# Kernel tuning notes

Hardware: AMD Instinct MI355X
Metric: run time of the kernel (lower is better)

Reference implementation:

```python
import jax, jax.numpy as jnp
import numpy as np

B, L, D_MODEL = 8, 2048, 768
D_INNER, D_STATE, DT_RANK, K = 1536, 16, 48, 4


def setup_inputs() -> dict:
    key = jax.random.key(0)
    ks = jax.random.split(key, 9)
    s = 0.02
    return {
        "hidden_states": jax.random.normal(ks[0], (B, L, D_MODEL), jnp.float32),
        "W_in": jax.random.normal(ks[1], (D_MODEL, 2 * D_INNER), jnp.float32) * s,
        "conv_w": jax.random.normal(ks[2], (D_INNER, 1, K), jnp.float32) * s,
        "conv_b": jax.random.normal(ks[3], (D_INNER,), jnp.float32) * s,
        "W_x": jax.random.normal(ks[4], (DT_RANK + 2 * D_STATE, D_INNER), jnp.float32) * s,
        "W_dt": jax.random.normal(ks[5], (D_INNER, DT_RANK), jnp.float32) * s,
        "b_dt": jax.random.normal(ks[6], (D_INNER,), jnp.float32) * s,
        "A_log": jax.random.normal(ks[7], (D_INNER, D_STATE), jnp.float32),
        "D_param": jax.random.normal(ks[8], (D_INNER,), jnp.float32),
    }


def _mamba(hidden_states, W_in, conv_w, conv_b, W_x, W_dt, b_dt, A_log, D_param):
    # in_proj then chunk into ssm branch (x) and gating residual (res)
    xz = hidden_states @ W_in                      # (B, L, 2*d_inner)
    x, res = jnp.split(xz, 2, axis=-1)             # each (B, L, d_inner)

    # causal depthwise conv over time, then SiLU
    xc = x.transpose(0, 2, 1)                      # (B, C, L)
    xc = jax.lax.conv_general_dilated(
        xc, conv_w, window_strides=(1,), padding=[(K - 1, 0)],
        feature_group_count=D_INNER, dimension_numbers=("NCH", "OIH", "NCH"))
    x = jax.nn.silu(xc + conv_b[None, :, None]).transpose(0, 2, 1)  # (B, L, d_inner)

    # input-dependent SSM parameters
    x_dbl = x @ W_x.T                              # (B, L, dt_rank + 2*d_state)
    dt = jax.nn.softplus(x_dbl[..., :DT_RANK] @ W_dt.T + b_dt)      # (B, L, d_inner)
    Bm = x_dbl[..., DT_RANK:DT_RANK + D_STATE]     # (B, L, d_state)
    Cm = x_dbl[..., DT_RANK + D_STATE:]            # (B, L, d_state)
    A = -jnp.exp(A_log)                            # (d_inner, d_state)

    def step(h, inp):
        x_t, dt_t, B_t, C_t = inp                  # (B,d_inner),(B,d_inner),(B,d_state),(B,d_state)
        dA = jnp.exp(dt_t[..., None] * A)          # (B, d_inner, d_state)
        dBx = (dt_t * x_t)[..., None] * B_t[:, None, :]
        h = dA * h + dBx
        y = jnp.einsum("bds,bs->bd", h, C_t)
        return h, y

    xs = (x.transpose(1, 0, 2), dt.transpose(1, 0, 2),
          Bm.transpose(1, 0, 2), Cm.transpose(1, 0, 2))
    h0 = jnp.zeros((x.shape[0], D_INNER, D_STATE), x.dtype)
    _, ys = jax.lax.scan(step, h0, xs)             # ys: (L, B, d_inner)
    y = ys.transpose(1, 0, 2) + x * D_param        # skip term
    return y * jax.nn.silu(res)                    # gated output (B, L, d_inner)


def reference(hidden_states, W_in, conv_w, conv_b, W_x, W_dt, b_dt, A_log, D_param):
    return _mamba(hidden_states, W_in, conv_w, conv_b, W_x, W_dt, b_dt, A_log, D_param)
```

## Files before the change

### kernel.cpp

```cpp
#include <hip/hip_runtime.h>
#include <hip/hip_bf16.h>
#include <stdint.h>

#define B_SZ 8
#define L_SZ 2048
#define DM 768
#define DI 1536
#define DS 16
#define DR 48
#define M_SZ (B_SZ * L_SZ)
#define N1 (2 * DI)

#define NC 32
#define TC (L_SZ / NC)
#define CH (B_SZ * DI)
#define KS 6
#define NT2 (DM / 32)
#define L2E 1.44269504088896f

typedef short short8 __attribute__((ext_vector_type(8)));
typedef float f32x4 __attribute__((ext_vector_type(4)));
typedef float f32x2 __attribute__((ext_vector_type(2)));

__device__ __forceinline__ ushort f2b(float f) {
  __hip_bfloat16 h = __float2bfloat16(f);
  return *reinterpret_cast<ushort*>(&h);
}
__device__ __forceinline__ float b2f(ushort u) {
  __hip_bfloat16 h;
  *reinterpret_cast<ushort*>(&h) = u;
  return __bfloat162float(h);
}
__device__ __forceinline__ ushort f2h(float f) {
  _Float16 h = (_Float16)f;
  return *reinterpret_cast<ushort*>(&h);
}
__device__ __forceinline__ float h2f(ushort u) {
  _Float16 h;
  *reinterpret_cast<ushort*>(&h) = u;
  return (float)h;
}

__device__ __forceinline__ void gl16(const ushort* g, ushort* l) {
  __builtin_amdgcn_global_load_lds(
      (const __attribute__((address_space(1))) void*)g,
      (__attribute__((address_space(3))) void*)l, 16, 0, 0);
}


__global__ __launch_bounds__(256) void prep_all(const float4* __restrict__ hs4,
                                                const float* __restrict__ w_in,
                                                const float* __restrict__ wx_f,
                                                const float* __restrict__ wdt_f,
                                                ushort4* __restrict__ A1,
                                                ushort* __restrict__ wt,
                                                ushort* __restrict__ wx_b,
                                                ushort* __restrict__ wdt_p) {
  const int n4 = M_SZ * DM / 4;
  const int nT = 3072 * 96;
  const int nwx = 80 * DI;
  const int nwdt = DI * 64;
  int idx = blockIdx.x * 256 + threadIdx.x;
  if (idx < n4) {
    float4 v = hs4[idx];
    ushort4 o;
    o.x = f2b(v.x); o.y = f2b(v.y); o.z = f2b(v.z); o.w = f2b(v.w);
    A1[idx] = o;
  } else if (idx < n4 + nT) {
    int j = idx - n4;
    int n = j % 3072;
    int kb = (j / 3072) * 8;
    short8 o;
#pragma unroll
    for (int q = 0; q < 8; ++q) o[q] = (short)f2b(w_in[(size_t)(kb + q) * 3072 + n]);
    *(short8*)(wt + (size_t)n * DM + kb) = o;
  } else if (idx < n4 + nT + nwx) {
    int j = idx - n4 - nT;
    wx_b[j] = f2b(wx_f[j]);
  } else if (idx < n4 + nT + nwx + nwdt) {
    int j = idx - n4 - nT - nwx;
    int col = j >> 6, k = j & 63;
    wdt_p[j] = (k < DR) ? f2b(wdt_f[col * DR + k]) : (ushort)0;
  }
}


__global__ __launch_bounds__(512, 4) void gemm_xz(const ushort* __restrict__ A,
                                                  const ushort* __restrict__ Bt,
                                                  ushort* __restrict__ xout,
                                                  ushort* __restrict__ gateout) {
  __shared__ ushort lds[36864];

  const int t = threadIdx.x;
  const int lane = t & 63;
  const int wid = t >> 6;
  const int wm = wid >> 2, wn = wid & 3;
  const int r = lane & 15, hi = lane >> 4;

  const int g = blockIdx.x;
  const int swz = (g & 7) * 192 + (g >> 3);
  const int bx = swz & 63;
  const int by = swz >> 6;
  const int bm = bx * 256;
  const int bn = by * 128;

  const ushort* gsrc[3];
  int ldso[3];
#pragma unroll
  for (int i = 0; i < 3; ++i) {
    int c = wid * 3 + i;
    if (c < 16)
      gsrc[i] = A + (size_t)(bm + c * 16 + r) * DM + hi * 8;
    else
      gsrc[i] = Bt + (size_t)(bn + (c - 16) * 16 + r) * DM + hi * 8;
    ldso[i] = c * 512;
  }

  f32x4 acc[8][2];
#pragma unroll
  for (int m = 0; m < 8; ++m)
#pragma unroll
    for (int n = 0; n < 2; ++n) acc[m][n] = f32x4{0.f, 0.f, 0.f, 0.f};

  ushort* b0 = lds;
  ushort* b1 = lds + 12288;
  ushort* b2 = lds + 24576;

#pragma unroll
  for (int i = 0; i < 3; ++i) gl16(gsrc[i], b0 + ldso[i]);
#pragma unroll
  for (int i = 0; i < 3; ++i) gl16(gsrc[i] + 32, b1 + ldso[i]);
  asm volatile("s_waitcnt vmcnt(3)" ::: "memory");
  __builtin_amdgcn_s_barrier();

  for (int kt = 0; kt < NT2; ++kt) {
    const bool stage = (kt + 2 < NT2);
    const int koff = (kt + 2) * 32;

    short8 bfr[2];
#pragma unroll
    for (int n = 0; n < 2; ++n)
      bfr[n] = *(const short8*)&b0[(16 + wn * 2 + n) * 512 + lane * 8];

#pragma unroll
    for (int q = 0; q < 2; ++q) {
      short8 afr[4];
#pragma unroll
      for (int m = 0; m < 4; ++m)
        afr[m] = *(const short8*)&b0[(wm * 8 + q * 4 + m) * 512 + lane * 8];

      if (stage) {
        if (q == 0) {
          gl16(gsrc[0] + koff, b2 + ldso[0]);
          gl16(gsrc[1] + koff, b2 + ldso[1]);
        } else {
          gl16(gsrc[2] + koff, b2 + ldso[2]);
        }
      }

      asm volatile("s_barrier" ::: "memory");

      __builtin_amdgcn_s_setprio(1);
#pragma unroll
      for (int m = 0; m < 4; ++m)
#pragma unroll
        for (int n = 0; n < 2; ++n)
          acc[q * 4 + m][n] =
              __builtin_amdgcn_mfma_f32_16x16x32_bf16(afr[m], bfr[n], acc[q * 4 + m][n], 0, 0, 0);
      __builtin_amdgcn_s_setprio(0);

      if (q == 1) {
        if (stage)
          asm volatile("s_waitcnt vmcnt(3)" ::: "memory");
        else
          asm volatile("s_waitcnt vmcnt(0)" ::: "memory");
      }
      asm volatile("s_barrier" ::: "memory");
    }

    ushort* tmp = b0; b0 = b1; b1 = b2; b2 = tmp;
  }

  const bool isx = (bn < DI);
  ushort* outp = isx ? xout : gateout;
  const int cbase = bn - (isx ? 0 : DI) + wn * 32;
#pragma unroll
  for (int mf = 0; mf < 8; ++mf)
#pragma unroll
    for (int nf = 0; nf < 2; ++nf) {
      int col = cbase + nf * 16 + r;
#pragma unroll
      for (int j = 0; j < 4; ++j) {
        int row = bm + wm * 128 + mf * 16 + hi * 4 + j;
        float v = acc[mf][nf][j];
        if (!isx) v = v / (1.f + __expf(-v));
        outp[(size_t)row * DI + col] = f2b(v);
      }
    }
}


__global__ __launch_bounds__(256) void conv_silu(const ushort* __restrict__ xp,
                                                 const float* __restrict__ cw,
                                                 const float* __restrict__ cb,
                                                 ushort* __restrict__ xc) {
  int tid = blockIdx.x * 256 + threadIdx.x;
  const int nd = DI / 8;
  int db = tid % nd;
  int row = tid / nd;
  int d0 = db * 8;
  int l = row & (L_SZ - 1);
  const ushort* base = xp + (size_t)row * DI + d0;
  short8 z8 = {0, 0, 0, 0, 0, 0, 0, 0};
  short8 x0 = *(const short8*)base;
  short8 xm1 = (l >= 1) ? *(const short8*)(base - DI) : z8;
  short8 xm2 = (l >= 2) ? *(const short8*)(base - 2 * DI) : z8;
  short8 xm3 = (l >= 3) ? *(const short8*)(base - 3 * DI) : z8;
  short8 o;
#pragma unroll
  for (int j = 0; j < 8; ++j) {
    float4 w = *(const float4*)(cw + (size_t)(d0 + j) * 4);
    float a = cb[d0 + j] + w.x * b2f((ushort)xm3[j]) + w.y * b2f((ushort)xm2[j]) +
              w.z * b2f((ushort)xm1[j]) + w.w * b2f((ushort)x0[j]);
    float s = a / (1.f + __expf(-a));
    o[j] = (short)f2b(s);
  }
  *(short8*)(xc + (size_t)row * DI + d0) = o;
}


__global__ __launch_bounds__(256) void xdbl_gemm(const ushort* __restrict__ xc,
                                                 const ushort* __restrict__ wx,
                                                 float* __restrict__ xdp) {
  int wave = blockIdx.x * 4 + (threadIdx.x >> 6);
  int ks = blockIdx.y;
  int lane = threadIdx.x & 63;
  int r = lane & 15, hi = lane >> 4;
  int row0 = wave * 16;
  f32x4 acc[5];
#pragma unroll
  for (int n = 0; n < 5; ++n) acc[n] = f32x4{0.f, 0.f, 0.f, 0.f};
  const int kbeg = ks * (DI / KS), kend = kbeg + DI / KS;
  for (int k0 = kbeg; k0 < kend; k0 += 32) {
    short8 a = *(const short8*)(xc + (size_t)(row0 + r) * DI + k0 + hi * 8);
#pragma unroll
    for (int n = 0; n < 5; ++n) {
      short8 b = *(const short8*)(wx + (size_t)(n * 16 + r) * DI + k0 + hi * 8);
      acc[n] = __builtin_amdgcn_mfma_f32_16x16x32_bf16(a, b, acc[n], 0, 0, 0);
    }
  }
  float* op = xdp + (size_t)ks * M_SZ * 80;
#pragma unroll
  for (int n = 0; n < 5; ++n)
#pragma unroll
    for (int j = 0; j < 4; ++j)
      op[(size_t)(row0 + hi * 4 + j) * 80 + n * 16 + r] = acc[n][j];
}

__global__ __launch_bounds__(256) void reduce_xd(const float4* __restrict__ xdp,
                                                 float4* __restrict__ xd) {
  int i = blockIdx.x * 256 + threadIdx.x;
  if (i >= M_SZ * 20) return;
  float4 s = xdp[i];
#pragma unroll
  for (int k = 1; k < KS; ++k) {
    float4 v = xdp[(size_t)k * M_SZ * 20 + i];
    s.x += v.x; s.y += v.y; s.z += v.z; s.w += v.w;
  }
  xd[i] = s;
}


__device__ __forceinline__ short8 pack8f(const float* p) {
  short8 v;
#pragma unroll
  for (int i = 0; i < 8; ++i) v[i] = (short)f2b(p[i]);
  return v;
}

__global__ __launch_bounds__(256) void dt_gemm(const float* __restrict__ xd,
                                               const ushort* __restrict__ wdtp,
                                               const float* __restrict__ bdt,
                                               ushort* __restrict__ dt) {
  int wave = blockIdx.x * 4 + (threadIdx.x >> 6);
  int lane = threadIdx.x & 63;
  int r = lane & 15, hi = lane >> 4;
  int row0 = wave * 16;
  int c0 = blockIdx.y * 64;

  float atmp[8];
  const float* ap = xd + (size_t)(row0 + r) * 80 + hi * 8;
  float4 q0 = *(const float4*)ap, q1 = *(const float4*)(ap + 4);
  atmp[0] = q0.x; atmp[1] = q0.y; atmp[2] = q0.z; atmp[3] = q0.w;
  atmp[4] = q1.x; atmp[5] = q1.y; atmp[6] = q1.z; atmp[7] = q1.w;
  short8 a0 = pack8f(atmp);
  short8 a1 = {0, 0, 0, 0, 0, 0, 0, 0};
  if (hi < 2) {
    const float* ap1 = xd + (size_t)(row0 + r) * 80 + 32 + hi * 8;
    float4 p0 = *(const float4*)ap1, p1 = *(const float4*)(ap1 + 4);
    atmp[0] = p0.x; atmp[1] = p0.y; atmp[2] = p0.z; atmp[3] = p0.w;
    atmp[4] = p1.x; atmp[5] = p1.y; atmp[6] = p1.z; atmp[7] = p1.w;
    a1 = pack8f(atmp);
  }

  f32x4 acc[4];
#pragma unroll
  for (int n = 0; n < 4; ++n) acc[n] = f32x4{0.f, 0.f, 0.f, 0.f};
#pragma unroll
  for (int n = 0; n < 4; ++n) {
    const ushort* wp = wdtp + (size_t)(c0 + n * 16 + r) * 64;
    short8 b0 = *(const short8*)(wp + hi * 8);
    short8 b1 = *(const short8*)(wp + 32 + hi * 8);
    acc[n] = __builtin_amdgcn_mfma_f32_16x16x32_bf16(a0, b0, acc[n], 0, 0, 0);
    acc[n] = __builtin_amdgcn_mfma_f32_16x16x32_bf16(a1, b1, acc[n], 0, 0, 0);
  }
#pragma unroll
  for (int n = 0; n < 4; ++n)
#pragma unroll
    for (int j = 0; j < 4; ++j) {
      int col = c0 + n * 16 + r;
      float z = acc[n][j] + bdt[col];
      float sp = (z > 20.f) ? z : __logf(1.f + __expf(z));
      dt[(size_t)(row0 + hi * 4 + j) * DI + col] = f2h(sp);
    }
}


__global__ __launch_bounds__(256) void scan_pass1(const ushort* __restrict__ dt,
                                                  const ushort* __restrict__ xc,
                                                  const float* __restrict__ xd,
                                                  const float* __restrict__ A_log,
                                                  float* __restrict__ hend,
                                                  float* __restrict__ sumdt) {
  const int d = blockIdx.x * 256 + threadIdx.x;
  const int c = blockIdx.y, b = blockIdx.z;
  const int t0 = c * TC;

  __shared__ float Bs[TC * 16];
  for (int i = threadIdx.x; i < TC * 16; i += 256) {
    int tt = i >> 4, s = i & 15;
    Bs[i] = xd[((size_t)(b * L_SZ + t0 + tt)) * 80 + DR + s];
  }

  f32x2 a2[8];
  const float4* al4 = (const float4*)(A_log + (size_t)d * DS);
#pragma unroll
  for (int q = 0; q < 4; ++q) {
    float4 v = al4[q];
    a2[2 * q] = f32x2{-__expf(v.x) * L2E, -__expf(v.y) * L2E};
    a2[2 * q + 1] = f32x2{-__expf(v.z) * L2E, -__expf(v.w) * L2E};
  }

  __syncthreads();

  f32x2 h2[8];
#pragma unroll
  for (int q = 0; q < 8; ++q) h2[q] = f32x2{0.f, 0.f};
  float sd = 0.f;

  const ushort* dtp = dt + ((size_t)b * L_SZ + t0) * DI + d;
  const ushort* xp = xc + ((size_t)b * L_SZ + t0) * DI + d;

  ushort dtu_n = *dtp;
  ushort xu_n = *xp;
  const f32x2* bp2 = (const f32x2*)Bs;
#pragma unroll 2
  for (int tt = 0; tt < TC; ++tt) {
    dtp += DI; xp += DI;
    ushort dtu = dtu_n;
    ushort xu = xu_n;
    dtu_n = *dtp;
    xu_n = *xp;
    float dtv = h2f(dtu);
    float xv = b2f(xu);
    sd += dtv;
    float dx = dtv * xv;
    f32x2 dts = f32x2{dtv, dtv};
    f32x2 dxs = f32x2{dx, dx};
#pragma unroll
    for (int q = 0; q < 8; ++q) {
      f32x2 bv = bp2[q];
      f32x2 arg, t2;
      asm("v_pk_mul_f32 %0, %1, %2" : "=v"(arg) : "v"(dts), "v"(a2[q]));
      float e0, e1;
      asm("v_exp_f32 %0, %1" : "=v"(e0) : "v"(arg[0]));
      asm("v_exp_f32 %0, %1" : "=v"(e1) : "v"(arg[1]));
      asm("v_pk_mul_f32 %0, %1, %2" : "=v"(t2) : "v"(dxs), "v"(bv));
      h2[q][0] = __builtin_fmaf(e0, h2[q][0], t2[0]);
      h2[q][1] = __builtin_fmaf(e1, h2[q][1], t2[1]);
    }
    bp2 += 8;
  }

  const size_t ch = (size_t)b * DI + d;
  sumdt[ch * NC + c] = sd;
  f32x2* hp = (f32x2*)&hend[((size_t)c * CH + ch) * 16];
#pragma unroll
  for (int q = 0; q < 8; ++q) hp[q] = h2[q];
}

__global__ __launch_bounds__(256) void scan_pass2(const float* __restrict__ A_log,
                                                  const float* __restrict__ sumdt,
                                                  const float* __restrict__ hend,
                                                  float* __restrict__ hstart) {
  int idx = blockIdx.x * 256 + threadIdx.x;
  int ch = idx >> 4, s = idx & 15;
  int d = ch % DI;
  float A = -__expf(A_log[d * DS + s]);
  float h = 0.f;
  for (int c = 0; c < NC; ++c) {
    hstart[((size_t)c * CH + ch) * 16 + s] = h;
    float sd = sumdt[(size_t)ch * NC + c];
    h = __expf(A * sd) * h + hend[((size_t)c * CH + ch) * 16 + s];
  }
}

__global__ __launch_bounds__(256) void scan_pass3(const ushort* __restrict__ dt,
                                                  const ushort* __restrict__ xc,
                                                  const float* __restrict__ xd,
                                                  const ushort* __restrict__ gateb,
                                                  const float* __restrict__ A_log,
                                                  const float* __restrict__ Dp,
                                                  const float* __restrict__ hstart,
                                                  float* __restrict__ out) {
  const int d = blockIdx.x * 256 + threadIdx.x;
  const int c = blockIdx.y, b = blockIdx.z;
  const int t0 = c * TC;

  __shared__ float Bs[TC * 16];
  __shared__ float Cs[TC * 16];
  for (int i = threadIdx.x; i < TC * 16; i += 256) {
    int tt = i >> 4, s = i & 15;
    size_t row = ((size_t)(b * L_SZ + t0 + tt)) * 80;
    Bs[i] = xd[row + DR + s];
    Cs[i] = xd[row + DR + DS + s];
  }

  f32x2 a2[8];
  const float4* al4 = (const float4*)(A_log + (size_t)d * DS);
#pragma unroll
  for (int q = 0; q < 4; ++q) {
    float4 v = al4[q];
    a2[2 * q] = f32x2{-__expf(v.x) * L2E, -__expf(v.y) * L2E};
    a2[2 * q + 1] = f32x2{-__expf(v.z) * L2E, -__expf(v.w) * L2E};
  }
  const float Dpv = Dp[d];

  const size_t ch = (size_t)b * DI + d;
  f32x2 h2[8];
  const f32x2* hp = (const f32x2*)&hstart[((size_t)c * CH + ch) * 16];
#pragma unroll
  for (int q = 0; q < 8; ++q) h2[q] = hp[q];

  __syncthreads();

  const ushort* dtp = dt + ((size_t)b * L_SZ + t0) * DI + d;
  const ushort* xp = xc + ((size_t)b * L_SZ + t0) * DI + d;
  const ushort* gp = gateb + ((size_t)b * L_SZ + t0) * DI + d;
  float* op = out + ((size_t)b * L_SZ + t0) * DI + d;

  ushort dtu_n = *dtp;
  ushort xu_n = *xp;
  ushort gu_n = *gp;
  const f32x2* bp2 = (const f32x2*)Bs;
  const f32x2* cp2 = (const f32x2*)Cs;
#pragma unroll 2
  for (int tt = 0; tt < TC; ++tt) {
    dtp += DI; xp += DI; gp += DI;
    ushort dtu = dtu_n;
    ushort xu = xu_n;
    ushort gu = gu_n;
    dtu_n = *dtp;
    xu_n = *xp;
    gu_n = *gp;
    float dtv = h2f(dtu);
    float xv = b2f(xu);
    float gv = b2f(gu);
    float dx = dtv * xv;
    f32x2 dts = f32x2{dtv, dtv};
    f32x2 dxs = f32x2{dx, dx};
    f32x2 ya = f32x2{0.f, 0.f}, yb = f32x2{0.f, 0.f};
#pragma unroll
    for (int q = 0; q < 8; ++q) {
      f32x2 bv = bp2[q];
      f32x2 cv = cp2[q];
      f32x2 arg, t2;
      asm("v_pk_mul_f32 %0, %1, %2" : "=v"(arg) : "v"(dts), "v"(a2[q]));
      float e0, e1;
      asm("v_exp_f32 %0, %1" : "=v"(e0) : "v"(arg[0]));
      asm("v_exp_f32 %0, %1" : "=v"(e1) : "v"(arg[1]));
      asm("v_pk_mul_f32 %0, %1, %2" : "=v"(t2) : "v"(dxs), "v"(bv));
      h2[q][0] = __builtin_fmaf(e0, h2[q][0], t2[0]);
      h2[q][1] = __builtin_fmaf(e1, h2[q][1], t2[1]);
      if (q & 1)
        asm("v_pk_fma_f32 %0, %1, %2, %0" : "+v"(yb) : "v"(h2[q]), "v"(cv));
      else
        asm("v_pk_fma_f32 %0, %1, %2, %0" : "+v"(ya) : "v"(h2[q]), "v"(cv));
    }
    bp2 += 8; cp2 += 8;
    float y = (ya[0] + ya[1]) + (yb[0] + yb[1]);
    op[0] = (y + xv * Dpv) * gv;
    op += DI;
  }
}


extern "C" void kernel_launch(void* const* d_in, const int* in_sizes, int n_in,
                              void* d_out, int out_size, void* d_ws, size_t ws_size,
                              hipStream_t stream) {
  const float* hs     = (const float*)d_in[0];
  const float* W_in   = (const float*)d_in[1];
  const float* conv_w = (const float*)d_in[2];
  const float* conv_b = (const float*)d_in[3];
  const float* W_x    = (const float*)d_in[4];
  const float* W_dt   = (const float*)d_in[5];
  const float* b_dt   = (const float*)d_in[6];
  const float* A_log  = (const float*)d_in[7];
  const float* D_par  = (const float*)d_in[8];
  float* out = (float*)d_out;
  char* ws = (char*)d_ws;

  size_t o = 0;
  ushort* A1   = (ushort*)(ws + o); o += (size_t)M_SZ * DM * 2;
  ushort* Wt1  = (ushort*)(ws + o); o += (size_t)N1 * DM * 2;
  ushort* xpre = (ushort*)(ws + o); o += (size_t)M_SZ * DI * 2;
  ushort* gate = (ushort*)(ws + o); o += (size_t)M_SZ * DI * 2;
  ushort* xcv  = (ushort*)(ws + o); o += (size_t)M_SZ * DI * 2;
  float*  xdbl = (float*)(ws + o);  o += (size_t)M_SZ * 80 * 4;
  ushort* dtb  = (ushort*)(ws + o); o += (size_t)M_SZ * DI * 2;
  float*  xdp  = (float*)(ws + o);  o += (size_t)KS * M_SZ * 80 * 4;
  ushort* Wxb  = (ushort*)(ws + o); o += (size_t)80 * DI * 2;
  ushort* Wdtp = (ushort*)(ws + o); o += (size_t)DI * 64 * 2;
  if (ws_size < o) return;

  float* hend   = (float*)(ws + 0);
  float* hstart = (float*)(ws + (size_t)NC * CH * 16 * 4);
  float* sumdt  = (float*)(ws + (size_t)2 * NC * CH * 16 * 4);

  const int nprep = M_SZ * DM / 4 + 3072 * 96 + 80 * DI + DI * 64;
  prep_all<<<dim3((nprep + 255) / 256), dim3(256), 0, stream>>>(
      (const float4*)hs, W_in, W_x, W_dt, (ushort4*)A1, Wt1, Wxb, Wdtp);

  gemm_xz<<<dim3((M_SZ / 256) * (N1 / 128)), dim3(512), 0, stream>>>(A1, Wt1, xpre, gate);

  conv_silu<<<dim3(M_SZ * DI / 8 / 256), dim3(256), 0, stream>>>(xpre, conv_w, conv_b, xcv);

  xdbl_gemm<<<dim3(M_SZ / 64, KS), dim3(256), 0, stream>>>(xcv, Wxb, xdp);
  reduce_xd<<<dim3((M_SZ * 20 + 255) / 256), dim3(256), 0, stream>>>((const float4*)xdp, (float4*)xdbl);

  dt_gemm<<<dim3(M_SZ / 64, 24), dim3(256), 0, stream>>>(xdbl, Wdtp, b_dt, dtb);

  scan_pass1<<<dim3(DI / 256, NC, B_SZ), dim3(256), 0, stream>>>(dtb, xcv, xdbl, A_log, hend, sumdt);
  scan_pass2<<<dim3(CH * 16 / 256), dim3(256), 0, stream>>>(A_log, sumdt, hend, hstart);
  scan_pass3<<<dim3(DI / 256, NC, B_SZ), dim3(256), 0, stream>>>(dtb, xcv, xdbl, gate,
                                                                 A_log, D_par, hstart, out);
}
```

Measured before the change: 447.7 us.

## Enlarge in-projection GEMM tile to 256x256 and vectorize scan B/C LDS reads

The in-projection GEMM tile grows from 256x128 to 256x256, with more LDS, four loads per thread per stage and a new XCD-aware block mapping. Launch bounds drop to one block per CU. The goal is more operand reuse per LDS load and less global traffic, at the cost of higher register pressure, lower occupancy and half as many blocks. The scan passes also read B and C from LDS as float4 instead of float2, to cut the number of LDS instructions.

```diff
diff --git a/kernel.cpp b/kernel.cpp
--- a/kernel.cpp
+++ b/kernel.cpp
@@ -85,11 +85,11 @@
 }
 
 
-__global__ __launch_bounds__(512, 4) void gemm_xz(const ushort* __restrict__ A,
+__global__ __launch_bounds__(512, 1) void gemm_xz(const ushort* __restrict__ A,
                                                   const ushort* __restrict__ Bt,
                                                   ushort* __restrict__ xout,
                                                   ushort* __restrict__ gateout) {
-  __shared__ ushort lds[36864];
+  __shared__ ushort lds[49152];
 
   const int t = threadIdx.x;
   const int lane = t & 63;
@@ -98,17 +98,18 @@
   const int r = lane & 15, hi = lane >> 4;
 
   const int g = blockIdx.x;
-  const int swz = (g & 7) * 192 + (g >> 3);
-  const int bx = swz & 63;
-  const int by = swz >> 6;
+  const int xcd = g & 7;
+  const int local = g >> 3;
+  const int bx = xcd * 8 + local / 12;
+  const int by = local % 12;
   const int bm = bx * 256;
-  const int bn = by * 128;
-
-  const ushort* gsrc[3];
-  int ldso[3];
-#pragma unroll
-  for (int i = 0; i < 3; ++i) {
-    int c = wid * 3 + i;
+  const int bn = by * 256;
+
+  const ushort* gsrc[4];
+  int ldso[4];
+#pragma unroll
+  for (int i = 0; i < 4; ++i) {
+    int c = wid * 4 + i;
     if (c < 16)
       gsrc[i] = A + (size_t)(bm + c * 16 + r) * DM + hi * 8;
     else
@@ -116,31 +117,31 @@
     ldso[i] = c * 512;
   }
 
-  f32x4 acc[8][2];
+  f32x4 acc[8][4];
 #pragma unroll
   for (int m = 0; m < 8; ++m)
 #pragma unroll
-    for (int n = 0; n < 2; ++n) acc[m][n] = f32x4{0.f, 0.f, 0.f, 0.f};
+    for (int n = 0; n < 4; ++n) acc[m][n] = f32x4{0.f, 0.f, 0.f, 0.f};
 
   ushort* b0 = lds;
-  ushort* b1 = lds + 12288;
-  ushort* b2 = lds + 24576;
-
-#pragma unroll
-  for (int i = 0; i < 3; ++i) gl16(gsrc[i], b0 + ldso[i]);
-#pragma unroll
-  for (int i = 0; i < 3; ++i) gl16(gsrc[i] + 32, b1 + ldso[i]);
-  asm volatile("s_waitcnt vmcnt(3)" ::: "memory");
+  ushort* b1 = lds + 16384;
+  ushort* b2 = lds + 32768;
+
+#pragma unroll
+  for (int i = 0; i < 4; ++i) gl16(gsrc[i], b0 + ldso[i]);
+#pragma unroll
+  for (int i = 0; i < 4; ++i) gl16(gsrc[i] + 32, b1 + ldso[i]);
+  asm volatile("s_waitcnt vmcnt(4)" ::: "memory");
   __builtin_amdgcn_s_barrier();
 
   for (int kt = 0; kt < NT2; ++kt) {
     const bool stage = (kt + 2 < NT2);
     const int koff = (kt + 2) * 32;
 
-    short8 bfr[2];
-#pragma unroll
-    for (int n = 0; n < 2; ++n)
-      bfr[n] = *(const short8*)&b0[(16 + wn * 2 + n) * 512 + lane * 8];
+    short8 bfr[4];
+#pragma unroll
+    for (int n = 0; n < 4; ++n)
+      bfr[n] = *(const short8*)&b0[(16 + wn * 4 + n) * 512 + lane * 8];
 
 #pragma unroll
     for (int q = 0; q < 2; ++q) {
@@ -150,12 +151,8 @@
         afr[m] = *(const short8*)&b0[(wm * 8 + q * 4 + m) * 512 + lane * 8];
 
       if (stage) {
-        if (q == 0) {
-          gl16(gsrc[0] + koff, b2 + ldso[0]);
-          gl16(gsrc[1] + koff, b2 + ldso[1]);
-        } else {
-          gl16(gsrc[2] + koff, b2 + ldso[2]);
-        }
+        gl16(gsrc[2 * q] + koff, b2 + ldso[2 * q]);
+        gl16(gsrc[2 * q + 1] + koff, b2 + ldso[2 * q + 1]);
       }
 
       asm volatile("s_barrier" ::: "memory");
@@ -164,14 +161,14 @@
 #pragma unroll
       for (int m = 0; m < 4; ++m)
 #pragma unroll
-        for (int n = 0; n < 2; ++n)
+        for (int n = 0; n < 4; ++n)
           acc[q * 4 + m][n] =
               __builtin_amdgcn_mfma_f32_16x16x32_bf16(afr[m], bfr[n], acc[q * 4 + m][n], 0, 0, 0);
       __builtin_amdgcn_s_setprio(0);
 
       if (q == 1) {
         if (stage)
-          asm volatile("s_waitcnt vmcnt(3)" ::: "memory");
+          asm volatile("s_waitcnt vmcnt(4)" ::: "memory");
         else
           asm volatile("s_waitcnt vmcnt(0)" ::: "memory");
       }
@@ -183,11 +180,11 @@
 
   const bool isx = (bn < DI);
   ushort* outp = isx ? xout : gateout;
-  const int cbase = bn - (isx ? 0 : DI) + wn * 32;
+  const int cbase = bn - (isx ? 0 : DI) + wn * 64;
 #pragma unroll
   for (int mf = 0; mf < 8; ++mf)
 #pragma unroll
-    for (int nf = 0; nf < 2; ++nf) {
+    for (int nf = 0; nf < 4; ++nf) {
       int col = cbase + nf * 16 + r;
 #pragma unroll
       for (int j = 0; j < 4; ++j) {
@@ -363,7 +360,7 @@
 
   ushort dtu_n = *dtp;
   ushort xu_n = *xp;
-  const f32x2* bp2 = (const f32x2*)Bs;
+  const f32x4* bp4 = (const f32x4*)Bs;
 #pragma unroll 2
   for (int tt = 0; tt < TC; ++tt) {
     dtp += DI; xp += DI;
@@ -378,18 +375,23 @@
     f32x2 dts = f32x2{dtv, dtv};
     f32x2 dxs = f32x2{dx, dx};
 #pragma unroll
-    for (int q = 0; q < 8; ++q) {
-      f32x2 bv = bp2[q];
-      f32x2 arg, t2;
-      asm("v_pk_mul_f32 %0, %1, %2" : "=v"(arg) : "v"(dts), "v"(a2[q]));
-      float e0, e1;
-      asm("v_exp_f32 %0, %1" : "=v"(e0) : "v"(arg[0]));
-      asm("v_exp_f32 %0, %1" : "=v"(e1) : "v"(arg[1]));
-      asm("v_pk_mul_f32 %0, %1, %2" : "=v"(t2) : "v"(dxs), "v"(bv));
-      h2[q][0] = __builtin_fmaf(e0, h2[q][0], t2[0]);
-      h2[q][1] = __builtin_fmaf(e1, h2[q][1], t2[1]);
+    for (int q4 = 0; q4 < 4; ++q4) {
+      f32x4 bq = bp4[q4];
+#pragma unroll
+      for (int hq = 0; hq < 2; ++hq) {
+        int q = q4 * 2 + hq;
+        f32x2 bv = f32x2{bq[2 * hq], bq[2 * hq + 1]};
+        f32x2 arg, t2;
+        asm("v_pk_mul_f32 %0, %1, %2" : "=v"(arg) : "v"(dts), "v"(a2[q]));
+        float e0, e1;
+        asm("v_exp_f32 %0, %1" : "=v"(e0) : "v"(arg[0]));
+        asm("v_exp_f32 %0, %1" : "=v"(e1) : "v"(arg[1]));
+        asm("v_pk_mul_f32 %0, %1, %2" : "=v"(t2) : "v"(dxs), "v"(bv));
+        h2[q][0] = __builtin_fmaf(e0, h2[q][0], t2[0]);
+        h2[q][1] = __builtin_fmaf(e1, h2[q][1], t2[1]);
+      }
     }
-    bp2 += 8;
+    bp4 += 4;
   }
 
   const size_t ch = (size_t)b * DI + d;
@@ -462,8 +464,8 @@
   ushort dtu_n = *dtp;
   ushort xu_n = *xp;
   ushort gu_n = *gp;
-  const f32x2* bp2 = (const f32x2*)Bs;
-  const f32x2* cp2 = (const f32x2*)Cs;
+  const f32x4* bp4 = (const f32x4*)Bs;
+  const f32x4* cp4 = (const f32x4*)Cs;
 #pragma unroll 2
   for (int tt = 0; tt < TC; ++tt) {
     dtp += DI; xp += DI; gp += DI;
@@ -481,23 +483,29 @@
     f32x2 dxs = f32x2{dx, dx};
     f32x2 ya = f32x2{0.f, 0.f}, yb = f32x2{0.f, 0.f};
 #pragma unroll
-    for (int q = 0; q < 8; ++q) {
-      f32x2 bv = bp2[q];
-      f32x2 cv = cp2[q];
-      f32x2 arg, t2;
-      asm("v_pk_mul_f32 %0, %1, %2" : "=v"(arg) : "v"(dts), "v"(a2[q]));
-      float e0, e1;
-      asm("v_exp_f32 %0, %1" : "=v"(e0) : "v"(arg[0]));
-      asm("v_exp_f32 %0, %1" : "=v"(e1) : "v"(arg[1]));
-      asm("v_pk_mul_f32 %0, %1, %2" : "=v"(t2) : "v"(dxs), "v"(bv));
-      h2[q][0] = __builtin_fmaf(e0, h2[q][0], t2[0]);
-      h2[q][1] = __builtin_fmaf(e1, h2[q][1], t2[1]);
-      if (q & 1)
-        asm("v_pk_fma_f32 %0, %1, %2, %0" : "+v"(yb) : "v"(h2[q]), "v"(cv));
-      else
-        asm("v_pk_fma_f32 %0, %1, %2, %0" : "+v"(ya) : "v"(h2[q]), "v"(cv));
+    for (int q4 = 0; q4 < 4; ++q4) {
+      f32x4 bq = bp4[q4];
+      f32x4 cq = cp4[q4];
+#pragma unroll
+      for (int hq = 0; hq < 2; ++hq) {
+        int q = q4 * 2 + hq;
+        f32x2 bv = f32x2{bq[2 * hq], bq[2 * hq + 1]};
+        f32x2 cv = f32x2{cq[2 * hq], cq[2 * hq + 1]};
+        f32x2 arg, t2;
+        asm("v_pk_mul_f32 %0, %1, %2" : "=v"(arg) : "v"(dts), "v"(a2[q]));
+        float e0, e1;
+        asm("v_exp_f32 %0, %1" : "=v"(e0) : "v"(arg[0]));
+        asm("v_exp_f32 %0, %1" : "=v"(e1) : "v"(arg[1]));
+        asm("v_pk_mul_f32 %0, %1, %2" : "=v"(t2) : "v"(dxs), "v"(bv));
+        h2[q][0] = __builtin_fmaf(e0, h2[q][0], t2[0]);
+        h2[q][1] = __builtin_fmaf(e1, h2[q][1], t2[1]);
+        if (hq)
+          asm("v_pk_fma_f32 %0, %1, %2, %0" : "+v"(yb) : "v"(h2[q]), "v"(cv));
+        else
+          asm("v_pk_fma_f32 %0, %1, %2, %0" : "+v"(ya) : "v"(h2[q]), "v"(cv));
+      }
     }
-    bp2 += 8; cp2 += 8;
+    bp4 += 4; cp4 += 4;
     float y = (ya[0] + ya[1]) + (yb[0] + yb[1]);
     op[0] = (y + xv * Dpv) * gv;
     op += DI;
@@ -541,7 +549,7 @@
   prep_all<<<dim3((nprep + 255) / 256), dim3(256), 0, stream>>>(
       (const float4*)hs, W_in, W_x, W_dt, (ushort4*)A1, Wt1, Wxb, Wdtp);
 
-  gemm_xz<<<dim3((M_SZ / 256) * (N1 / 128)), dim3(512), 0, stream>>>(A1, Wt1, xpre, gate);
+  gemm_xz<<<dim3((M_SZ / 256) * (N1 / 256)), dim3(512), 0, stream>>>(A1, Wt1, xpre, gate);
 
   conv_silu<<<dim3(M_SZ * DI / 8 / 256), dim3(256), 0, stream>>>(xpre, conv_w, conv_b, xcv);
 
```

After: 415.9 us. -7.1%, faster.
